# Kernel optimization log

Hardware: AMD Instinct MI355X
Metric: run time of the kernel (lower is better)

## Reference

```python
import jax, jax.numpy as jnp
import numpy as np
from jax import nn as jnn

N = 100000      # nodes
E = 3200000     # edges (avg degree 32)
G = 1024        # graphs in batch
F_IN = 3        # num_features (hard-coded in module)
D = 32          # dim (hard-coded in module)
BN_EPS = 1e-5


def setup_inputs() -> dict:
    key = jax.random.key(0)
    ks = jax.random.split(key, 24)
    def lin(k, i, o):
        return (jax.random.normal(k, (i, o), jnp.float32) / np.sqrt(i)).astype(jnp.float32)
    inp = {}
    inp["x"] = jax.random.normal(ks[0], (N, F_IN), jnp.float32)
    inp["edge_index"] = jax.random.randint(ks[1], (2, E), 0, N, dtype=jnp.int32)
    inp["batch"] = jnp.sort(jax.random.randint(ks[2], (N,), 0, G, dtype=jnp.int32))
    idx = 3
    in_dims = [F_IN, D, D]
    for l in (1, 2, 3):
        inp[f"W{l}a"] = lin(ks[idx], in_dims[l - 1], D); idx += 1
        inp[f"b{l}a"] = jnp.zeros((D,), jnp.float32)
        inp[f"W{l}b"] = lin(ks[idx], D, D); idx += 1
        inp[f"b{l}b"] = jnp.zeros((D,), jnp.float32)
        inp[f"g{l}"] = jnp.ones((D,), jnp.float32)            # BN gamma
        inp[f"be{l}"] = jnp.zeros((D,), jnp.float32)          # BN beta
        inp[f"m{l}"] = 0.1 * jax.random.normal(ks[idx], (D,), jnp.float32); idx += 1  # running mean
        inp[f"v{l}"] = jax.random.uniform(ks[idx], (D,), jnp.float32, 0.5, 1.5); idx += 1  # running var
    inp["Wf1"] = lin(ks[idx], D, D); idx += 1
    inp["bf1"] = jnp.zeros((D,), jnp.float32)
    inp["Wf2"] = lin(ks[idx], D, 1)
    inp["bf2"] = jnp.zeros((1,), jnp.float32)
    return inp


def reference(x, edge_index, batch,
              W1a, b1a, W1b, b1b, g1, be1, m1, v1,
              W2a, b2a, W2b, b2b, g2, be2, m2, v2,
              W3a, b3a, W3b, b3b, g3, be3, m3, v3,
              Wf1, bf1, Wf2, bf2):
    src, dst = edge_index[0], edge_index[1]

    def gin_bn(h, Wa, ba, Wb, bb, g, be, m, v):
        # GINConv (eps=0): nn(x + sum_{j->i} x_j); then relu; then BatchNorm1d (eval stats)
        agg = jax.ops.segment_sum(h[src], dst, num_segments=N) + h  # [N, d]
        h2 = jnn.relu(agg @ Wa + ba) @ Wb + bb                      # 2-layer MLP
        h2 = jnn.relu(h2)
        return g * (h2 - m) * jax.lax.rsqrt(v + BN_EPS) + be

    h = gin_bn(x, W1a, b1a, W1b, b1b, g1, be1, m1, v1)
    h = gin_bn(h, W2a, b2a, W2b, b2b, g2, be2, m2, v2)
    h = gin_bn(h, W3a, b3a, W3b, b3b, g3, be3, m3, v3)
    p = jax.ops.segment_sum(h, batch, num_segments=G)   # global_add_pool -> [G, D]
    p = jnn.relu(p @ Wf1 + bf1)
    # dropout p=0.5 is identity at inference
    return jnp.tanh(p @ Wf2 + bf2)                      # [G, 1]
```

## Files before the change

### kernel.cpp

```cpp
#include <hip/hip_runtime.h>
#include <math.h>

#define D 32
#define BN_EPS 1e-5f
#define NRANGE 512
#define RWC 196
#define MAXD 80
#define EPB 8192
#define K1_TPB 512
#define EPT (EPB / K1_TPB)
#define PCH 8

__global__ __launch_bounds__(K1_TPB) void build_part(
    const int* __restrict__ src, const int* __restrict__ dst,
    unsigned int* __restrict__ part, int* __restrict__ gcount,
    int E, int cap, int RW, unsigned long long M) {
    __shared__ unsigned int sorted[EPB];
    __shared__ unsigned short rid[EPB];
    __shared__ int cnt[NRANGE];
    __shared__ int exc[NRANGE];
    __shared__ int cur[NRANGE];
    __shared__ int gbase[NRANGE];
    int t = threadIdx.x;
    cnt[t] = 0;
    __syncthreads();

    int base = blockIdx.x * EPB;
    int n = min(EPB, E - base);

    unsigned int mypk[EPT];
    unsigned short myr[EPT];
#pragma unroll
    for (int k = 0; k < EPT; k++) {
        int i = t + k * K1_TPB;
        if (i < n) {
            int d = dst[base + i];
            int s = src[base + i];
            int r = (int)(((unsigned long long)d * M) >> 40);
            mypk[k] = ((unsigned)(d - r * RW) << 17) | (unsigned)s;
            myr[k] = (unsigned short)r;
            atomicAdd(&cnt[r], 1);
        } else myr[k] = 0xFFFFu;
    }
    __syncthreads();

    int inc = cnt[t];
    exc[t] = inc;
    __syncthreads();
    for (int s = 1; s < NRANGE; s <<= 1) {
        int u = (t >= s) ? exc[t - s] : 0;
        __syncthreads();
        exc[t] += u;
        __syncthreads();
    }
    int excl = exc[t] - cnt[t];
    __syncthreads();
    exc[t] = excl;
    cur[t] = excl;
    gbase[t] = atomicAdd(&gcount[t], cnt[t]);
    __syncthreads();

#pragma unroll
    for (int k = 0; k < EPT; k++) {
        if (myr[k] != 0xFFFFu) {
            int j = atomicAdd(&cur[myr[k]], 1);
            sorted[j] = mypk[k];
            rid[j] = myr[k];
        }
    }
    __syncthreads();

    for (int j = t; j < n; j += K1_TPB) {
        int r = rid[j];
        int pos = gbase[r] + (j - exc[r]);
        if (pos < cap) part[(size_t)r * cap + pos] = sorted[j];
    }
}

__global__ __launch_bounds__(1024) void build_csr(
    const unsigned int* __restrict__ part, const int* __restrict__ gcount,
    int* __restrict__ col, int* __restrict__ deg,
    int cap, int RW, int N, int maxd) {
    __shared__ int bucket[RWC * MAXD];
    __shared__ int rank_[RWC];
    int r = blockIdx.x, t = threadIdx.x, T = blockDim.x;
    for (int i = t; i < RW; i += T) rank_[i] = 0;
    __syncthreads();

    int count = gcount[r]; if (count > cap) count = cap;
    const unsigned int* p = part + (size_t)r * cap;
    int nbase = r * RW;
    for (int i = t; i < count; i += T) {
        unsigned int v = p[i];
        int dl = (int)(v >> 17);
        int slot = atomicAdd(&rank_[dl], 1);
        if (slot < maxd) bucket[dl * maxd + slot] = (int)(v & 0x1FFFFu);
    }
    __syncthreads();

    for (int i = t; i < RW; i += T) {
        int rk = rank_[i]; if (rk > maxd) rk = maxd;
        int pdg = (rk + 15) & ~15; if (pdg > maxd) pdg = maxd;
        int self = nbase + i;
        for (int k = rk; k < pdg; k++) bucket[i * maxd + k] = self;
    }
    __syncthreads();

    int nvalid = N - nbase; if (nvalid > RW) nvalid = RW;
    if (nvalid <= 0) return;
    int words = nvalid * maxd;
    int4* dst4 = (int4*)&col[(size_t)nbase * maxd];
    const int4* src4 = (const int4*)bucket;
    int nq = words >> 2;
    for (int i = t; i < nq; i += T) dst4[i] = src4[i];
    for (int i = t; i < nvalid; i += T) {
        int rk = rank_[i];
        deg[nbase + i] = rk < maxd ? rk : maxd;
    }
}

__global__ void compute_y(const float* __restrict__ x, const float* __restrict__ W1a,
                          float* __restrict__ y, int N) {
    long long gid = (long long)blockIdx.x * blockDim.x + threadIdx.x;
    int i = (int)(gid >> 5);
    int lane = (int)(gid & 31);
    if (i >= N) return;
    float x0 = x[i * 3 + 0], x1 = x[i * 3 + 1], x2 = x[i * 3 + 2];
    float t = x0 * W1a[0 * D + lane];
    t = fmaf(x1, W1a[1 * D + lane], t);
    t = fmaf(x2, W1a[2 * D + lane], t);
    y[(size_t)i * D + lane] = t;
}

template <bool SKIP_WA>
__global__ void layer_fused(const float* __restrict__ hin, const int* __restrict__ deg,
                            const int* __restrict__ col, int maxd,
                            const float* __restrict__ Wa, const float* __restrict__ ba,
                            const float* __restrict__ Wb, const float* __restrict__ bb,
                            const float* __restrict__ g, const float* __restrict__ be,
                            const float* __restrict__ m, const float* __restrict__ v,
                            float* __restrict__ hout, int N) {
    long long gid = (long long)blockIdx.x * blockDim.x + threadIdx.x;
    int i = (int)(gid >> 5);
    int lane = (int)(gid & 31);
    if (i >= N) return;

    int dg = deg[i];
    if (dg > maxd) dg = maxd;
    int pdg = (dg + 15) & ~15; if (pdg > maxd) pdg = maxd;
    float acc = hin[(size_t)i * D + lane] * (float)(1 + dg - pdg);
    const int* cp = &col[(size_t)i * maxd];
    int e = 0;
    for (; e + 32 <= pdg; e += 32) {
        int4 c0 = *(const int4*)&cp[e];
        int4 c1 = *(const int4*)&cp[e + 4];
        int4 c2 = *(const int4*)&cp[e + 8];
        int4 c3 = *(const int4*)&cp[e + 12];
        int4 c4 = *(const int4*)&cp[e + 16];
        int4 c5 = *(const int4*)&cp[e + 20];
        int4 c6 = *(const int4*)&cp[e + 24];
        int4 c7 = *(const int4*)&cp[e + 28];
        float a0 = hin[(size_t)c0.x * D + lane];
        float a1 = hin[(size_t)c0.y * D + lane];
        float a2 = hin[(size_t)c0.z * D + lane];
        float a3 = hin[(size_t)c0.w * D + lane];
        float a4 = hin[(size_t)c1.x * D + lane];
        float a5 = hin[(size_t)c1.y * D + lane];
        float a6 = hin[(size_t)c1.z * D + lane];
        float a7 = hin[(size_t)c1.w * D + lane];
        float a8 = hin[(size_t)c2.x * D + lane];
        float a9 = hin[(size_t)c2.y * D + lane];
        float a10 = hin[(size_t)c2.z * D + lane];
        float a11 = hin[(size_t)c2.w * D + lane];
        float a12 = hin[(size_t)c3.x * D + lane];
        float a13 = hin[(size_t)c3.y * D + lane];
        float a14 = hin[(size_t)c3.z * D + lane];
        float a15 = hin[(size_t)c3.w * D + lane];
        float a16 = hin[(size_t)c4.x * D + lane];
        float a17 = hin[(size_t)c4.y * D + lane];
        float a18 = hin[(size_t)c4.z * D + lane];
        float a19 = hin[(size_t)c4.w * D + lane];
        float a20 = hin[(size_t)c5.x * D + lane];
        float a21 = hin[(size_t)c5.y * D + lane];
        float a22 = hin[(size_t)c5.z * D + lane];
        float a23 = hin[(size_t)c5.w * D + lane];
        float a24 = hin[(size_t)c6.x * D + lane];
        float a25 = hin[(size_t)c6.y * D + lane];
        float a26 = hin[(size_t)c6.z * D + lane];
        float a27 = hin[(size_t)c6.w * D + lane];
        float a28 = hin[(size_t)c7.x * D + lane];
        float a29 = hin[(size_t)c7.y * D + lane];
        float a30 = hin[(size_t)c7.z * D + lane];
        float a31 = hin[(size_t)c7.w * D + lane];
        acc += (((a0 + a1) + (a2 + a3)) + ((a4 + a5) + (a6 + a7))) +
               (((a8 + a9) + (a10 + a11)) + ((a12 + a13) + (a14 + a15))) +
               (((a16 + a17) + (a18 + a19)) + ((a20 + a21) + (a22 + a23))) +
               (((a24 + a25) + (a26 + a27)) + ((a28 + a29) + (a30 + a31)));
    }
    for (; e + 16 <= pdg; e += 16) {
        int4 c0 = *(const int4*)&cp[e];
        int4 c1 = *(const int4*)&cp[e + 4];
        int4 c2 = *(const int4*)&cp[e + 8];
        int4 c3 = *(const int4*)&cp[e + 12];
        float a0 = hin[(size_t)c0.x * D + lane];
        float a1 = hin[(size_t)c0.y * D + lane];
        float a2 = hin[(size_t)c0.z * D + lane];
        float a3 = hin[(size_t)c0.w * D + lane];
        float a4 = hin[(size_t)c1.x * D + lane];
        float a5 = hin[(size_t)c1.y * D + lane];
        float a6 = hin[(size_t)c1.z * D + lane];
        float a7 = hin[(size_t)c1.w * D + lane];
        float a8 = hin[(size_t)c2.x * D + lane];
        float a9 = hin[(size_t)c2.y * D + lane];
        float aa = hin[(size_t)c2.z * D + lane];
        float ab = hin[(size_t)c2.w * D + lane];
        float ac = hin[(size_t)c3.x * D + lane];
        float ad = hin[(size_t)c3.y * D + lane];
        float ae = hin[(size_t)c3.z * D + lane];
        float af = hin[(size_t)c3.w * D + lane];
        acc += ((a0 + a1) + (a2 + a3)) + ((a4 + a5) + (a6 + a7)) +
               (((a8 + a9) + (aa + ab)) + ((ac + ad) + (ae + af)));
    }

    float t;
    if (SKIP_WA) {
        t = fmaxf(acc + ba[lane], 0.f);
    } else {
        t = ba[lane];
#pragma unroll
        for (int k = 0; k < D; k++) {
            float ak = __shfl(acc, k, D);
            t = fmaf(ak, Wa[k * D + lane], t);
        }
        t = fmaxf(t, 0.f);
    }
    float o = bb[lane];
#pragma unroll
    for (int j = 0; j < D; j++) {
        float tj = __shfl(t, j, D);
        o = fmaf(tj, Wb[j * D + lane], o);
    }
    o = fmaxf(o, 0.f);
    hout[(size_t)i * D + lane] =
        g[lane] * (o - m[lane]) * rsqrtf(v[lane] + BN_EPS) + be[lane];
}

__device__ __forceinline__ int lower_bound_i(const int* a, int n, int key) {
    int lo = 0, hi = n;
    while (lo < hi) {
        int mid = (lo + hi) >> 1;
        if (a[mid] < key) lo = mid + 1; else hi = mid;
    }
    return lo;
}

__global__ void pool_partial(const float* __restrict__ h, const int* __restrict__ batch,
                             float* __restrict__ pool, int N, int G) {
    long long gid = (long long)blockIdx.x * blockDim.x + threadIdx.x;
    int grp = (int)(gid >> 5);
    int lane = (int)(gid & 31);
    int gi = grp / PCH;
    int c = grp - gi * PCH;
    if (gi >= G) return;
    int lo = lower_bound_i(batch, N, gi);
    int hi = lower_bound_i(batch, N, gi + 1);
    int len = hi - lo;
    if (len <= 0) return;
    int chunk = (len + PCH - 1) / PCH;
    int s = lo + c * chunk;
    int e = s + chunk; if (e > hi) e = hi;
    if (s >= e) return;
    float p = 0.f;
    for (int n = s; n < e; n++) p += h[(size_t)n * D + lane];
    atomicAdd(&pool[(size_t)gi * D + lane], p);
}

__global__ void head_kernel(const float* __restrict__ pool, const float* __restrict__ Wf1,
                            const float* __restrict__ bf1, const float* __restrict__ Wf2,
                            const float* __restrict__ bf2, float* __restrict__ out, int G) {
    long long gid = (long long)blockIdx.x * blockDim.x + threadIdx.x;
    int gi = (int)(gid >> 5);
    int lane = (int)(gid & 31);
    if (gi >= G) return;
    float p = pool[(size_t)gi * D + lane];
    float q = bf1[lane];
#pragma unroll
    for (int j = 0; j < D; j++) {
        float pj = __shfl(p, j, D);
        q = fmaf(pj, Wf1[j * D + lane], q);
    }
    q = fmaxf(q, 0.f);
    float r = q * Wf2[lane];
#pragma unroll
    for (int off = 16; off; off >>= 1) r += __shfl_xor(r, off, D);
    if (lane == 0) out[gi] = tanhf(r + bf2[0]);
}

extern "C" void kernel_launch(void* const* d_in, const int* in_sizes, int n_in,
                              void* d_out, int out_size, void* d_ws, size_t ws_size,
                              hipStream_t stream) {
    const float* x = (const float*)d_in[0];
    const int* ei = (const int*)d_in[1];
    const int* batch = (const int*)d_in[2];
    const int E = in_sizes[1] / 2;
    const int N = in_sizes[2];
    const int G = out_size;
    const int* src = ei;
    const int* dst = ei + E;

    const float* P[3][8];
    for (int l = 0; l < 3; l++)
        for (int k = 0; k < 8; k++) P[l][k] = (const float*)d_in[3 + 8 * l + k];
    const float* Wf1 = (const float*)d_in[27];
    const float* bf1 = (const float*)d_in[28];
    const float* Wf2 = (const float*)d_in[29];
    const float* bf2 = (const float*)d_in[30];

    const int RW = (N + NRANGE - 1) / NRANGE;
    const unsigned long long M = ((1ull << 40) + RW - 1) / RW;
    int mean = (E + NRANGE - 1) / NRANGE;
    int cap = mean + mean / 8 + 64;
    cap = (cap + 7) & ~7;

    float* ws = (float*)d_ws;
    size_t off = 0;
    float* h0 = ws + off; off += (size_t)N * D;
    float* h1 = ws + off; off += (size_t)N * D;
    unsigned int* part = (unsigned int*)h0;
    int* deg = (int*)(ws + off); off += N;
    int* gcount = (int*)(ws + off); off += NRANGE;
    float* pool = ws + off; off += (size_t)G * D;
    int* col = (int*)(ws + off);
    size_t remaining = ws_size / 4 > off ? ws_size / 4 - off : 0;
    int maxd = (int)(remaining / (size_t)N);
    if (maxd > MAXD) maxd = MAXD;
    maxd &= ~15;
    if (maxd < 16) maxd = 16;

    const int B = 256;
    long long tN32 = (long long)N * D;
    int nbp = (E + EPB - 1) / EPB;

    hipMemsetAsync(gcount, 0, NRANGE * sizeof(int), stream);
    build_part<<<nbp, K1_TPB, 0, stream>>>(src, dst, part, gcount, E, cap, RW, M);
    build_csr<<<NRANGE, 1024, 0, stream>>>(part, gcount, col, deg, cap, RW, N, maxd);

    compute_y<<<(int)((tN32 + B - 1) / B), B, 0, stream>>>(x, P[0][0], h0, N);
    layer_fused<true><<<(int)((tN32 + B - 1) / B), B, 0, stream>>>(
        h0, deg, col, maxd, P[0][0], P[0][1], P[0][2], P[0][3],
        P[0][4], P[0][5], P[0][6], P[0][7], h1, N);

    layer_fused<false><<<(int)((tN32 + B - 1) / B), B, 0, stream>>>(
        h1, deg, col, maxd, P[1][0], P[1][1], P[1][2], P[1][3],
        P[1][4], P[1][5], P[1][6], P[1][7], h0, N);

    layer_fused<false><<<(int)((tN32 + B - 1) / B), B, 0, stream>>>(
        h0, deg, col, maxd, P[2][0], P[2][1], P[2][2], P[2][3],
        P[2][4], P[2][5], P[2][6], P[2][7], h1, N);

    hipMemsetAsync(pool, 0, (size_t)G * D * sizeof(float), stream);
    pool_partial<<<(int)(((long long)G * PCH * 32 + B - 1) / B), B, 0, stream>>>(
        h1, batch, pool, N, G);
    head_kernel<<<(int)(((long long)G * D + B - 1) / B), B, 0, stream>>>(
        pool, Wf1, bf1, Wf2, bf2, (float*)d_out, G);
}
```

Before: 361.0 us.

## Fuse input projection into CSR build, use wave-shuffle scan, merge memsets

Replaces the shared-memory Hillis-Steele scan in build_part with a wavefront shuffle scan plus a small per-wave combine, cutting block barriers. Halves the edges per block in build_part to get more blocks. Moves the first-layer x@W1a projection into build_csr so compute_y is no longer a separate launch. Gives the partition buffer its own workspace region, since h0 is now written during build_csr, and zeroes gcount and pool with a single memset. The memset covering pool assumes pool sits directly after gcount in the workspace, which holds in the current layout.

```diff
diff --git a/kernel.cpp b/kernel.cpp
--- a/kernel.cpp
+++ b/kernel.cpp
@@ -6,7 +6,7 @@
 #define NRANGE 512
 #define RWC 196
 #define MAXD 80
-#define EPB 8192
+#define EPB 4096
 #define K1_TPB 512
 #define EPT (EPB / K1_TPB)
 #define PCH 8
@@ -21,6 +21,7 @@
     __shared__ int exc[NRANGE];
     __shared__ int cur[NRANGE];
     __shared__ int gbase[NRANGE];
+    __shared__ int wsum[K1_TPB / 64];
     int t = threadIdx.x;
     cnt[t] = 0;
     __syncthreads();
@@ -45,16 +46,21 @@
     __syncthreads();
 
     int inc = cnt[t];
-    exc[t] = inc;
-    __syncthreads();
-    for (int s = 1; s < NRANGE; s <<= 1) {
-        int u = (t >= s) ? exc[t - s] : 0;
-        __syncthreads();
-        exc[t] += u;
-        __syncthreads();
-    }
-    int excl = exc[t] - cnt[t];
-    __syncthreads();
+    int v = inc;
+#pragma unroll
+    for (int s = 1; s < 64; s <<= 1) {
+        int u = __shfl_up(v, s, 64);
+        if ((t & 63) >= s) v += u;
+    }
+    if ((t & 63) == 63) wsum[t >> 6] = v;
+    __syncthreads();
+    if (t == 0) {
+        int acc = 0;
+#pragma unroll
+        for (int w = 0; w < K1_TPB / 64; w++) { int tmp = wsum[w]; wsum[w] = acc; acc += tmp; }
+    }
+    __syncthreads();
+    int excl = v - inc + wsum[t >> 6];
     exc[t] = excl;
     cur[t] = excl;
     gbase[t] = atomicAdd(&gcount[t], cnt[t]);
@@ -80,6 +86,7 @@
 __global__ __launch_bounds__(1024) void build_csr(
     const unsigned int* __restrict__ part, const int* __restrict__ gcount,
     int* __restrict__ col, int* __restrict__ deg,
+    const float* __restrict__ x, const float* __restrict__ W1a, float* __restrict__ y,
     int cap, int RW, int N, int maxd) {
     __shared__ int bucket[RWC * MAXD];
     __shared__ int rank_[RWC];
@@ -117,19 +124,16 @@
         int rk = rank_[i];
         deg[nbase + i] = rk < maxd ? rk : maxd;
     }
-}
-
-__global__ void compute_y(const float* __restrict__ x, const float* __restrict__ W1a,
-                          float* __restrict__ y, int N) {
-    long long gid = (long long)blockIdx.x * blockDim.x + threadIdx.x;
-    int i = (int)(gid >> 5);
-    int lane = (int)(gid & 31);
-    if (i >= N) return;
-    float x0 = x[i * 3 + 0], x1 = x[i * 3 + 1], x2 = x[i * 3 + 2];
-    float t = x0 * W1a[0 * D + lane];
-    t = fmaf(x1, W1a[1 * D + lane], t);
-    t = fmaf(x2, W1a[2 * D + lane], t);
-    y[(size_t)i * D + lane] = t;
+
+    int gidx = t >> 5, lane = t & 31;
+    for (int nl = gidx; nl < nvalid; nl += 32) {
+        int node = nbase + nl;
+        float x0 = x[node * 3 + 0], x1 = x[node * 3 + 1], x2 = x[node * 3 + 2];
+        float tv = x0 * W1a[0 * D + lane];
+        tv = fmaf(x1, W1a[1 * D + lane], tv);
+        tv = fmaf(x2, W1a[2 * D + lane], tv);
+        y[(size_t)node * D + lane] = tv;
+    }
 }
 
 template <bool SKIP_WA>
@@ -326,7 +330,7 @@
     size_t off = 0;
     float* h0 = ws + off; off += (size_t)N * D;
     float* h1 = ws + off; off += (size_t)N * D;
-    unsigned int* part = (unsigned int*)h0;
+    unsigned int* part = (unsigned int*)(ws + off); off += (size_t)NRANGE * cap;
     int* deg = (int*)(ws + off); off += N;
     int* gcount = (int*)(ws + off); off += NRANGE;
     float* pool = ws + off; off += (size_t)G * D;
@@ -341,11 +345,11 @@
     long long tN32 = (long long)N * D;
     int nbp = (E + EPB - 1) / EPB;
 
-    hipMemsetAsync(gcount, 0, NRANGE * sizeof(int), stream);
+    hipMemsetAsync(gcount, 0, (NRANGE + (size_t)G * D) * sizeof(int), stream);
     build_part<<<nbp, K1_TPB, 0, stream>>>(src, dst, part, gcount, E, cap, RW, M);
-    build_csr<<<NRANGE, 1024, 0, stream>>>(part, gcount, col, deg, cap, RW, N, maxd);
-
-    compute_y<<<(int)((tN32 + B - 1) / B), B, 0, stream>>>(x, P[0][0], h0, N);
+    build_csr<<<NRANGE, 1024, 0, stream>>>(part, gcount, col, deg, x, P[0][0], h0,
+                                           cap, RW, N, maxd);
+
     layer_fused<true><<<(int)((tN32 + B - 1) / B), B, 0, stream>>>(
         h0, deg, col, maxd, P[0][0], P[0][1], P[0][2], P[0][3],
         P[0][4], P[0][5], P[0][6], P[0][7], h1, N);
@@ -358,7 +362,6 @@
         h0, deg, col, maxd, P[2][0], P[2][1], P[2][2], P[2][3],
         P[2][4], P[2][5], P[2][6], P[2][7], h1, N);
 
-    hipMemsetAsync(pool, 0, (size_t)G * D * sizeof(float), stream);
     pool_partial<<<(int)(((long long)G * PCH * 32 + B - 1) / B), B, 0, stream>>>(
         h1, batch, pool, N, G);
     head_kernel<<<(int)(((long long)G * D + B - 1) / B), B, 0, stream>>>(
```

New measurement: 352.6 us. -2.3%, faster.
